# Kernel optimization log

Measured on AMD Instinct MI355X. Metric: run time of the kernel, lower is better.

The kernel has to match this reference:

```python
import jax, jax.numpy as jnp
import numpy as np

# Static cluster layout: B graphs, PER atoms each; first NIN are 'inside'
# (aux_ind==0), remaining NOUT are 'outside' periodic images (aux_ind==1).
B, PER, NIN, K = 256, 1024, 256, 32
NOUT = PER - NIN
N = B * PER
R = 6.0        # cutoff radius (Angstrom)
BOX = 32.0     # box side -> ~30 neighbors within R at this density


def setup_inputs() -> dict:
    key = jax.random.key(0)
    pos = jax.random.uniform(key, (N, 3), dtype=jnp.float32) * BOX
    batch = (jnp.arange(N, dtype=jnp.int32) // PER)
    aux_ind = ((jnp.arange(N, dtype=jnp.int32) % PER) >= NIN).astype(jnp.int32)
    return {"pos": pos, "batch": batch, "aux_ind": aux_ind}


def _select_neighbors(d, valid, k):
    """Pick up to k valid candidates per target, lowest candidate index first.
    d: [..., C] distances, valid: [..., C] bool. Returns (idx, mask, dist),
    each [..., k]; padded slots have mask=False and dist=0."""
    C = d.shape[-1]
    order_key = jnp.where(valid, jnp.arange(C, dtype=jnp.int32), C + 1)
    idx = jnp.argsort(order_key, axis=-1)[..., :k]          # [..., k]
    mask = jnp.take_along_axis(valid, idx, axis=-1)
    dist = jnp.where(mask, jnp.take_along_axis(d, idx, axis=-1), 0.0)
    return idx.astype(jnp.int32), mask, dist


def reference(pos, batch, aux_ind):
    # batch/aux_ind are encoded by the static contiguous layout above;
    # they parameterize the same structure torch builds via scatter_add/cumsum.
    pg = pos.reshape(B, PER, 3)
    ins = pg[:, :NIN]            # [B, NIN, 3]  inside (target + intra-conv) nodes
    outs = pg[:, NIN:]           # [B, NOUT, 3] outside (inter-conv) nodes

    # intra edges: inside -> inside, same graph, no self loops
    d_ii = jnp.sqrt(jnp.sum((ins[:, :, None, :] - ins[:, None, :, :]) ** 2, -1))  # [B,NIN,NIN]
    valid_ii = (d_ii < R) & ~jnp.eye(NIN, dtype=bool)
    idx_ii, m_ii, dist_ii = _select_neighbors(d_ii, valid_ii, K)

    # inter edges: outside -> inside, same graph
    d_io = jnp.sqrt(jnp.sum((ins[:, :, None, :] - outs[:, None, :, :]) ** 2, -1))  # [B,NIN,NOUT]
    valid_io = d_io < R
    idx_io, m_io, dist_io = _select_neighbors(d_io, valid_io, K)

    # relabel to global node indices (flow='source_to_target': row=source, col=target)
    goff = (jnp.arange(B, dtype=jnp.int32) * PER)[:, None, None]       # [B,1,1]
    tgt = jnp.broadcast_to(goff + jnp.arange(NIN, dtype=jnp.int32)[None, :, None],
                           (B, NIN, K))
    src_ii = goff + idx_ii
    src_io = goff + NIN + idx_io

    edge_index = jnp.stack([src_ii.reshape(-1), tgt.reshape(-1)], 0)        # [2, B*NIN*K]
    edge_index_inter = jnp.stack([src_io.reshape(-1), tgt.reshape(-1)], 0)  # [2, B*NIN*K]

    return (edge_index, m_ii.reshape(-1), dist_ii,
            edge_index_inter, m_io.reshape(-1), dist_io)
```

## Files before the change

### kernel.cpp

```cpp
#include <hip/hip_runtime.h>


constexpr int BB    = 256;
constexpr int PERN  = 1024;
constexpr int NINC  = 256;
constexpr int KK    = 32;
constexpr unsigned EE = 256u * 256u * 32u;

typedef float v2f __attribute__((ext_vector_type(2)));

__device__ __forceinline__ v2f pk_add(v2f a, v2f b) {
    v2f d; asm("v_pk_add_f32 %0, %1, %2" : "=v"(d) : "v"(a), "v"(b)); return d;
}
__device__ __forceinline__ v2f pk_mul(v2f a, v2f b) {
    v2f d; asm("v_pk_mul_f32 %0, %1, %2" : "=v"(d) : "v"(a), "v"(b)); return d;
}

__device__ __forceinline__ int prefix_lt(unsigned long long m) {
    return __builtin_amdgcn_mbcnt_hi((unsigned)(m >> 32),
           __builtin_amdgcn_mbcnt_lo((unsigned)m, 0u));
}

__global__ __launch_bounds__(1024) void mo3e_kernel(const float* __restrict__ pos,
                                                    float* __restrict__ out) {
    __shared__ float sq[3 * PERN];
    __shared__ int   slotbuf[16][64];

    const int b   = blockIdx.x >> 4;
    const int tid = threadIdx.x;
    const int w   = tid >> 6;
    const int l   = tid & 63;
    const int i   = __builtin_amdgcn_readfirstlane((blockIdx.x & 15) * 16 + w);

    {
        const float* gp = pos + (size_t)b * PERN * 3;
        const int fo = (((tid >> 7) << 6) | (tid & 63)) * 2 + ((tid >> 6) & 1);
        sq[fo]            = gp[tid * 3 + 0];
        sq[PERN + fo]     = gp[tid * 3 + 1];
        sq[2 * PERN + fo] = gp[tid * 3 + 2];
    }
    __syncthreads();

    const int fi = (((i >> 7) << 6) | (i & 63)) * 2 + ((i >> 6) & 1);
    const float xi = sq[fi], yi = sq[PERN + fi], zi = sq[2 * PERN + fi];
    const v2f nx = {-xi, -xi}, ny = {-yi, -yi}, nz = {-zi, -zi};

    const v2f* xq = (const v2f*)sq;
    const v2f* yq = (const v2f*)(sq + PERN);
    const v2f* zq = (const v2f*)(sq + 2 * PERN);

    int* slots = slotbuf[w];

    int S0ii;
    {
        unsigned long long msk[4];
        int cnt = 0;
#pragma unroll
        for (int p = 0; p < 2; ++p) {
            const v2f qx = xq[p * 64 + l], qy = yq[p * 64 + l], qz = zq[p * 64 + l];
            const v2f dx = pk_add(qx, nx), dy = pk_add(qy, ny), dz = pk_add(qz, nz);
            const v2f d2 = pk_add(pk_add(pk_mul(dx, dx), pk_mul(dy, dy)), pk_mul(dz, dz));
            const int ja = p * 128 + l, jb = ja + 64;
            const bool va = (d2.x < 36.0f) && (ja != i);
            const bool vb = (d2.y < 36.0f) && (jb != i);
            const unsigned long long ma = __ballot(va);
            {
                const int slot = cnt + prefix_lt(ma);
                if (va && slot < KK) slots[slot] = ja;
                cnt += __popcll(ma);
            }
            const unsigned long long mb = __ballot(vb);
            {
                const int slot = cnt + prefix_lt(mb);
                if (vb && slot < KK) slots[slot] = jb;
                cnt += __popcll(mb);
            }
            msk[2 * p] = ma;
            msk[2 * p + 1] = mb;
        }
        S0ii = cnt < KK ? cnt : KK;
        if (S0ii < KK) {
            int pc = S0ii;
#pragma unroll
            for (int g = 0; g < 4; ++g) {
                const unsigned long long inv = ~msk[g];
                const int slot = pc + prefix_lt(inv);
                if (((inv >> l) & 1ull) && slot < KK) slots[slot] = g * 64 + l;
                pc += __popcll(inv);
                if (pc >= KK) break;
            }
        }
    }

    int S0io;
    {
        unsigned long long msk[12];
        int cnt = 0;
#pragma unroll
        for (int p = 2; p < 8; ++p) {
            const v2f qx = xq[p * 64 + l], qy = yq[p * 64 + l], qz = zq[p * 64 + l];
            const v2f dx = pk_add(qx, nx), dy = pk_add(qy, ny), dz = pk_add(qz, nz);
            const v2f d2 = pk_add(pk_add(pk_mul(dx, dx), pk_mul(dy, dy)), pk_mul(dz, dz));
            const int ca = p * 128 + l, cb = ca + 64;
            const bool va = (d2.x < 36.0f);
            const bool vb = (d2.y < 36.0f);
            const unsigned long long ma = __ballot(va);
            {
                const int slot = cnt + prefix_lt(ma);
                if (va && slot < KK) slots[KK + slot] = ca;
                cnt += __popcll(ma);
            }
            const unsigned long long mb = __ballot(vb);
            {
                const int slot = cnt + prefix_lt(mb);
                if (vb && slot < KK) slots[KK + slot] = cb;
                cnt += __popcll(mb);
            }
            msk[2 * (p - 2)] = ma;
            msk[2 * (p - 2) + 1] = mb;
        }
        S0io = cnt < KK ? cnt : KK;
        if (S0io < KK) {
            int pc = S0io;
#pragma unroll
            for (int g = 0; g < 12; ++g) {
                const unsigned long long inv = ~msk[g];
                const int slot = pc + prefix_lt(inv);
                if (((inv >> l) & 1ull) && slot < KK) slots[KK + slot] = NINC + g * 64 + l;
                pc += __popcll(inv);
                if (pc >= KK) break;
            }
        }
    }

    {
        const int h = l >> 5;
        const int k = l & 31;
        const int idx = slots[l];
        const int fg = (((idx >> 7) << 6) | (idx & 63)) * 2 + ((idx >> 6) & 1);
        const float dxe = xi - sq[fg];
        const float dye = yi - sq[PERN + fg];
        const float dze = zi - sq[2 * PERN + fg];
        const float d2e = dxe * dxe + dye * dye + dze * dze;

        const int S0 = h ? S0io : S0ii;
        const bool mv = k < S0;
        const float dist = mv ? __builtin_amdgcn_sqrtf(d2e) : 0.0f;

        const int goff = b * PERN;
        const unsigned e0  = (unsigned)(b * NINC + i) * KK;
        const unsigned off = (h ? 4u * EE : 0u) + e0 + (unsigned)k;

        out[off]           = (float)(goff + idx);
        out[off + EE]      = (float)(goff + i);
        out[off + 2u * EE] = mv ? 1.0f : 0.0f;
        out[off + 3u * EE] = dist;
    }
}

extern "C" void kernel_launch(void* const* d_in, const int* in_sizes, int n_in,
                              void* d_out, int out_size, void* d_ws, size_t ws_size,
                              hipStream_t stream) {
    const float* pos = (const float*)d_in[0];
    float* out = (float*)d_out;

    mo3e_kernel<<<dim3(BB * 16), dim3(1024), 0, stream>>>(pos, out);
}
```

Measured before the change: 105.1 us.

## Use 256-thread blocks with AoS shared positions and branchless slot compaction

Shrinks each block to four wavefronts, each handling one target atom, and launches four times as many blocks. Positions are copied into shared memory as interleaved xyz using vectorized float4 loads, replacing the permuted planar layout. Candidate compaction writes unconditionally, sending invalid lanes to a dump region instead of using predicated stores. This targets occupancy and branch overhead, at the cost of each block reloading the full graph positions and stride-3 shared-memory reads that may conflict on banks.

Result: faster. 102.0 us (-3.0%).

```diff
diff --git a/kernel.cpp b/kernel.cpp
--- a/kernel.cpp
+++ b/kernel.cpp
@@ -1,11 +1,8 @@
 #include <hip/hip_runtime.h>
 
 
-constexpr int BB    = 256;
-constexpr int PERN  = 1024;
-constexpr int NINC  = 256;
-constexpr int KK    = 32;
-constexpr unsigned EE = 256u * 256u * 32u;
+constexpr int KK = 32;
+constexpr unsigned EE = 2097152u;
 
 typedef float v2f __attribute__((ext_vector_type(2)));
 
@@ -21,135 +18,141 @@
            __builtin_amdgcn_mbcnt_lo((unsigned)m, 0u));
 }
 
-__global__ __launch_bounds__(1024) void mo3e_kernel(const float* __restrict__ pos,
-                                                    float* __restrict__ out) {
-    __shared__ float sq[3 * PERN];
-    __shared__ int   slotbuf[16][64];
+__global__ __launch_bounds__(256) void mo3e_kernel(const float* __restrict__ pos,
+                                                   float* __restrict__ out) {
+    __shared__ float sq[3072];
+    __shared__ int   slotrow[4][128];
 
-    const int b   = blockIdx.x >> 4;
+    const int blk = blockIdx.x;
+    const int b   = blk >> 6;
     const int tid = threadIdx.x;
     const int w   = tid >> 6;
     const int l   = tid & 63;
-    const int i   = __builtin_amdgcn_readfirstlane((blockIdx.x & 15) * 16 + w);
+    const int i   = __builtin_amdgcn_readfirstlane(((blk & 63) << 2) | w);
 
     {
-        const float* gp = pos + (size_t)b * PERN * 3;
-        const int fo = (((tid >> 7) << 6) | (tid & 63)) * 2 + ((tid >> 6) & 1);
-        sq[fo]            = gp[tid * 3 + 0];
-        sq[PERN + fo]     = gp[tid * 3 + 1];
-        sq[2 * PERN + fo] = gp[tid * 3 + 2];
+        const float4* g4 = (const float4*)(pos + (size_t)b * 3072);
+        float4* s4 = (float4*)sq;
+        s4[tid      ] = g4[tid      ];
+        s4[tid + 256] = g4[tid + 256];
+        s4[tid + 512] = g4[tid + 512];
     }
     __syncthreads();
 
-    const int fi = (((i >> 7) << 6) | (i & 63)) * 2 + ((i >> 6) & 1);
-    const float xi = sq[fi], yi = sq[PERN + fi], zi = sq[2 * PERN + fi];
+    const float xi = sq[3 * i], yi = sq[3 * i + 1], zi = sq[3 * i + 2];
     const v2f nx = {-xi, -xi}, ny = {-yi, -yi}, nz = {-zi, -zi};
 
-    const v2f* xq = (const v2f*)sq;
-    const v2f* yq = (const v2f*)(sq + PERN);
-    const v2f* zq = (const v2f*)(sq + 2 * PERN);
+    int* __restrict__ row = slotrow[w];
+    const int dump = 64 + l;
 
-    int* slots = slotbuf[w];
+    unsigned long long msk[16];
+    int cii = 0, cio = 0;
+    int av = 3 * l;
 
-    int S0ii;
-    {
-        unsigned long long msk[4];
-        int cnt = 0;
 #pragma unroll
-        for (int p = 0; p < 2; ++p) {
-            const v2f qx = xq[p * 64 + l], qy = yq[p * 64 + l], qz = zq[p * 64 + l];
-            const v2f dx = pk_add(qx, nx), dy = pk_add(qy, ny), dz = pk_add(qz, nz);
-            const v2f d2 = pk_add(pk_add(pk_mul(dx, dx), pk_mul(dy, dy)), pk_mul(dz, dz));
-            const int ja = p * 128 + l, jb = ja + 64;
-            const bool va = (d2.x < 36.0f) && (ja != i);
-            const bool vb = (d2.y < 36.0f) && (jb != i);
-            const unsigned long long ma = __ballot(va);
-            {
-                const int slot = cnt + prefix_lt(ma);
-                if (va && slot < KK) slots[slot] = ja;
-                cnt += __popcll(ma);
-            }
-            const unsigned long long mb = __ballot(vb);
-            {
-                const int slot = cnt + prefix_lt(mb);
-                if (vb && slot < KK) slots[slot] = jb;
-                cnt += __popcll(mb);
-            }
-            msk[2 * p] = ma;
-            msk[2 * p + 1] = mb;
+    for (int it = 0; it < 2; ++it) {
+        const float xa = sq[av], ya = sq[av + 1], za = sq[av + 2];
+        const float xb = sq[av + 192], yb = sq[av + 193], zb = sq[av + 194];
+        av += 384;
+        const v2f qx = {xa, xb}, qy = {ya, yb}, qz = {za, zb};
+        const v2f dx = pk_add(qx, nx), dy = pk_add(qy, ny), dz = pk_add(qz, nz);
+        const v2f d2 = pk_add(pk_add(pk_mul(dx, dx), pk_mul(dy, dy)), pk_mul(dz, dz));
+        const int c0 = it * 128;
+        {
+            const bool va = (d2.x < 36.0f) & ((c0 + l) != i);
+            const unsigned long long m = __ballot(va);
+            msk[2 * it] = m;
+            int ent = cii + prefix_lt(m);
+            ent = ent < 127 ? ent : 127;
+            ent = va ? ent : dump;
+            row[ent] = c0 + l;
+            cii += __popcll(m);
         }
-        S0ii = cnt < KK ? cnt : KK;
-        if (S0ii < KK) {
-            int pc = S0ii;
+        {
+            const bool vb = (d2.y < 36.0f) & ((c0 + 64 + l) != i);
+            const unsigned long long m = __ballot(vb);
+            msk[2 * it + 1] = m;
+            int ent = cii + prefix_lt(m);
+            ent = ent < 127 ? ent : 127;
+            ent = vb ? ent : dump;
+            row[ent] = c0 + 64 + l;
+            cii += __popcll(m);
+        }
+    }
+    const int S0ii = cii < KK ? cii : KK;
+    if (cii < KK) {
+        int pc = cii;
 #pragma unroll
-            for (int g = 0; g < 4; ++g) {
-                const unsigned long long inv = ~msk[g];
-                const int slot = pc + prefix_lt(inv);
-                if (((inv >> l) & 1ull) && slot < KK) slots[slot] = g * 64 + l;
-                pc += __popcll(inv);
-                if (pc >= KK) break;
-            }
+        for (int g = 0; g < 4; ++g) {
+            const unsigned long long inv = ~msk[g];
+            const bool pm = (inv >> l) & 1ull;
+            int ent = pc + prefix_lt(inv);
+            ent = pm ? ent : dump;
+            row[ent] = g * 64 + l;
+            pc += __popcll(inv);
+            if (pc >= KK) break;
         }
     }
 
-    int S0io;
-    {
-        unsigned long long msk[12];
-        int cnt = 0;
 #pragma unroll
-        for (int p = 2; p < 8; ++p) {
-            const v2f qx = xq[p * 64 + l], qy = yq[p * 64 + l], qz = zq[p * 64 + l];
-            const v2f dx = pk_add(qx, nx), dy = pk_add(qy, ny), dz = pk_add(qz, nz);
-            const v2f d2 = pk_add(pk_add(pk_mul(dx, dx), pk_mul(dy, dy)), pk_mul(dz, dz));
-            const int ca = p * 128 + l, cb = ca + 64;
+    for (int it = 2; it < 8; ++it) {
+        const float xa = sq[av], ya = sq[av + 1], za = sq[av + 2];
+        const float xb = sq[av + 192], yb = sq[av + 193], zb = sq[av + 194];
+        av += 384;
+        const v2f qx = {xa, xb}, qy = {ya, yb}, qz = {za, zb};
+        const v2f dx = pk_add(qx, nx), dy = pk_add(qy, ny), dz = pk_add(qz, nz);
+        const v2f d2 = pk_add(pk_add(pk_mul(dx, dx), pk_mul(dy, dy)), pk_mul(dz, dz));
+        const int c0 = it * 128;
+        {
             const bool va = (d2.x < 36.0f);
+            const unsigned long long m = __ballot(va);
+            msk[2 * it] = m;
+            int ent = cio + prefix_lt(m);
+            ent = ent < 95 ? ent : 95;
+            ent = va ? ent + KK : dump;
+            row[ent] = c0 + l;
+            cio += __popcll(m);
+        }
+        {
             const bool vb = (d2.y < 36.0f);
-            const unsigned long long ma = __ballot(va);
-            {
-                const int slot = cnt + prefix_lt(ma);
-                if (va && slot < KK) slots[KK + slot] = ca;
-                cnt += __popcll(ma);
-            }
-            const unsigned long long mb = __ballot(vb);
-            {
-                const int slot = cnt + prefix_lt(mb);
-                if (vb && slot < KK) slots[KK + slot] = cb;
-                cnt += __popcll(mb);
-            }
-            msk[2 * (p - 2)] = ma;
-            msk[2 * (p - 2) + 1] = mb;
+            const unsigned long long m = __ballot(vb);
+            msk[2 * it + 1] = m;
+            int ent = cio + prefix_lt(m);
+            ent = ent < 95 ? ent : 95;
+            ent = vb ? ent + KK : dump;
+            row[ent] = c0 + 64 + l;
+            cio += __popcll(m);
         }
-        S0io = cnt < KK ? cnt : KK;
-        if (S0io < KK) {
-            int pc = S0io;
+    }
+    const int S0io = cio < KK ? cio : KK;
+    if (cio < KK) {
+        int pc = cio;
 #pragma unroll
-            for (int g = 0; g < 12; ++g) {
-                const unsigned long long inv = ~msk[g];
-                const int slot = pc + prefix_lt(inv);
-                if (((inv >> l) & 1ull) && slot < KK) slots[KK + slot] = NINC + g * 64 + l;
-                pc += __popcll(inv);
-                if (pc >= KK) break;
-            }
+        for (int g = 4; g < 16; ++g) {
+            const unsigned long long inv = ~msk[g];
+            const bool pm = (inv >> l) & 1ull;
+            int ent = pc + prefix_lt(inv);
+            ent = pm ? ent + KK : dump;
+            row[ent] = g * 64 + l;
+            pc += __popcll(inv);
+            if (pc >= KK) break;
         }
     }
 
     {
-        const int h = l >> 5;
-        const int k = l & 31;
-        const int idx = slots[l];
-        const int fg = (((idx >> 7) << 6) | (idx & 63)) * 2 + ((idx >> 6) & 1);
-        const float dxe = xi - sq[fg];
-        const float dye = yi - sq[PERN + fg];
-        const float dze = zi - sq[2 * PERN + fg];
-        const float d2e = dxe * dxe + dye * dye + dze * dze;
+        const int idx = row[l];
+        const float qx = sq[3 * idx], qy = sq[3 * idx + 1], qz = sq[3 * idx + 2];
+        const float ddx = xi - qx, ddy = yi - qy, ddz = zi - qz;
+        const float d2e = ddx * ddx + ddy * ddy + ddz * ddz;
 
-        const int S0 = h ? S0io : S0ii;
-        const bool mv = k < S0;
+        const bool isA = l < KK;
+        const int  S0  = isA ? S0ii : S0io;
+        const bool mv  = (l & 31) < S0;
         const float dist = mv ? __builtin_amdgcn_sqrtf(d2e) : 0.0f;
 
-        const int goff = b * PERN;
-        const unsigned e0  = (unsigned)(b * NINC + i) * KK;
-        const unsigned off = (h ? 4u * EE : 0u) + e0 + (unsigned)k;
+        const int goff = b * 1024;
+        const unsigned e0  = (unsigned)(b * 256 + i) * 32u;
+        const unsigned off = (isA ? 0u : 4u * EE - 32u) + e0 + (unsigned)l;
 
         out[off]           = (float)(goff + idx);
         out[off + EE]      = (float)(goff + i);
@@ -164,5 +167,5 @@
     const float* pos = (const float*)d_in[0];
     float* out = (float*)d_out;
 
-    mo3e_kernel<<<dim3(BB * 16), dim3(1024), 0, stream>>>(pos, out);
+    mo3e_kernel<<<dim3(256 * 64), dim3(256), 0, stream>>>(pos, out);
 }
```
